# Kernel optimization log

Measured on AMD Instinct MI355X. Metric: run time of the kernel, lower is better.

Reference implementation:

```python
import jax, jax.numpy as jnp
import numpy as np

D_MODEL = 1024
NUM_HEADS = 16
D_K = D_MODEL // NUM_HEADS


def setup_inputs() -> dict:
    key = jax.random.key(0)
    k_x, k_q, k_k, k_v, k_o = jax.random.split(key, 5)
    s = 1.0 / np.sqrt(D_MODEL)
    return {
        "x": jax.random.normal(k_x, (2, 2048, D_MODEL), dtype=jnp.float32),
        "W_q": jax.random.normal(k_q, (D_MODEL, D_MODEL), dtype=jnp.float32) * s,
        "W_k": jax.random.normal(k_k, (D_MODEL, D_MODEL), dtype=jnp.float32) * s,
        "W_v": jax.random.normal(k_v, (D_MODEL, D_MODEL), dtype=jnp.float32) * s,
        "W_o": jax.random.normal(k_o, (D_MODEL, D_MODEL), dtype=jnp.float32) * s,
    }


def reference(x, W_q, W_k, W_v, W_o):
    B, S, D = x.shape
    H, dk = NUM_HEADS, D_K
    # nn.Linear(y) = y @ W.T ; weights stored as (out, in)
    def proj(W):
        return (x @ W.T).reshape(B, S, H, dk).transpose(0, 2, 1, 3)  # (B,H,S,dk)
    Q, K, V = proj(W_q), proj(W_k), proj(W_v)
    scores = jnp.einsum("bhqd,bhkd->bhqk", Q, K) / np.sqrt(dk)  # (B,H,S,S)
    attn = jax.nn.softmax(scores, axis=-1)
    out = jnp.einsum("bhqk,bhkd->bhqd", attn, V)  # (B,H,S,dk)
    out = out.transpose(0, 2, 1, 3).reshape(B, S, D)
    return out @ W_o.T
```

## Files before the change

kernel.cpp:

```cpp
#include <hip/hip_runtime.h>
#include <hip/hip_bf16.h>

#define SEQ 2048
#define DM  1024
#define NH  16
#define DK  64
#define MROWS 4096

typedef __attribute__((ext_vector_type(8))) short short8;
typedef __attribute__((ext_vector_type(4))) short short4v;
typedef __attribute__((ext_vector_type(4))) float float4v;

__device__ __forceinline__ short f2bf(float f) {
  union { float f; unsigned u; } v; v.f = f;
  unsigned r = v.u + 0x7fffu + ((v.u >> 16) & 1u);
  return (short)(r >> 16);
}
__device__ __forceinline__ short f2bfu(float f) {
  union { float f; unsigned u; } v; v.f = f;
  return (short)((v.u + 0x8000u) >> 16);
}

__global__ __launch_bounds__(256) void cvt_kernel(
    const float* __restrict__ in, short* __restrict__ out) {
  int i = blockIdx.x * 256 + threadIdx.x;
  float4v f = ((const float4v*)in)[i];
  short4v s;
#pragma unroll
  for (int j = 0; j < 4; ++j) s[j] = f2bf(f[j]);
  ((short4v*)out)[i] = s;
}

__global__ __launch_bounds__(256) void cvt4_kernel(
    const float* __restrict__ a, const float* __restrict__ b,
    const float* __restrict__ c, const float* __restrict__ d,
    short* __restrict__ out) {
  const float* srcs[4] = {a, b, c, d};
  const float* s = srcs[blockIdx.y];
  int i = blockIdx.x * 256 + threadIdx.x;
  float4v f = ((const float4v*)s)[i];
  short4v sv;
#pragma unroll
  for (int j = 0; j < 4; ++j) sv[j] = f2bf(f[j]);
  ((short4v*)(out + (size_t)blockIdx.y * DM * DM))[i] = sv;
}

template<typename TC>
__global__ __launch_bounds__(256) void gemm_bt_kernel(
    const short* __restrict__ A, const short* __restrict__ Bw0,
    TC* __restrict__ C0, int M, int N, int K, size_t strB, size_t strC,
    short* __restrict__ vtOut)
{
  __shared__ __align__(16) short Al[2][128 * 72];
  __shared__ __align__(16) short Bl[2][128 * 72];
  const short* Bw = Bw0 + (size_t)blockIdx.z * strB;
  TC* C = C0 + (size_t)blockIdx.z * strC;

  const int tid  = threadIdx.x;
  const int lane = tid & 63, wave = tid >> 6;
  const int l16  = lane & 15, quad = lane >> 4;
  const int wm   = (wave >> 1) * 64, wn = (wave & 1) * 64;
  const int cm   = blockIdx.y * 128, cn = blockIdx.x * 128;

  float4v acc[4][4];
#pragma unroll
  for (int i = 0; i < 4; ++i)
#pragma unroll
    for (int j = 0; j < 4; ++j)
#pragma unroll
      for (int r = 0; r < 4; ++r) acc[i][j][r] = 0.f;

  const short* ag = A  + (size_t)cm * K;
  const short* bg = Bw + (size_t)cn * K;
  int rw[4];
#pragma unroll
  for (int it = 0; it < 4; ++it) rw[it] = (it * 256 + tid) >> 3;
  const int cl = (tid & 7) * 8;

  short8 ra[4], rb[4];
  auto loadG = [&](int k0) {
#pragma unroll
    for (int it = 0; it < 4; ++it) {
      ra[it] = *(const short8*)(ag + (size_t)rw[it] * K + k0 + cl);
      rb[it] = *(const short8*)(bg + (size_t)rw[it] * K + k0 + cl);
    }
  };
  auto writeL = [&](int buf) {
#pragma unroll
    for (int it = 0; it < 4; ++it) {
      *(short8*)&Al[buf][rw[it] * 72 + cl] = ra[it];
      *(short8*)&Bl[buf][rw[it] * 72 + cl] = rb[it];
    }
  };
  auto compute = [&](int buf) {
#pragma unroll
    for (int ks = 0; ks < 2; ++ks) {
      short8 af[4], bfr[4];
#pragma unroll
      for (int mi = 0; mi < 4; ++mi)
        af[mi] = *(const short8*)&Al[buf][(wm + mi*16 + l16) * 72 + ks*32 + quad*8];
#pragma unroll
      for (int ni = 0; ni < 4; ++ni)
        bfr[ni] = *(const short8*)&Bl[buf][(wn + ni*16 + l16) * 72 + ks*32 + quad*8];
#pragma unroll
      for (int mi = 0; mi < 4; ++mi)
#pragma unroll
        for (int ni = 0; ni < 4; ++ni)
          acc[mi][ni] = __builtin_amdgcn_mfma_f32_16x16x32_bf16(
              af[mi], bfr[ni], acc[mi][ni], 0, 0, 0);
    }
  };

  loadG(0);
  writeL(0);
  __syncthreads();
  int cur = 0;
  for (int k0 = 0; k0 < K; k0 += 64) {
    bool nxt = (k0 + 64 < K);
    if (nxt) loadG(k0 + 64);
    compute(cur);
    if (nxt) writeL(cur ^ 1);
    __syncthreads();
    cur ^= 1;
  }

  if (vtOut != nullptr && blockIdx.z == 2) {
    short* T = &Al[0][0];
#pragma unroll
    for (int mi = 0; mi < 4; ++mi)
#pragma unroll
      for (int ni = 0; ni < 4; ++ni)
#pragma unroll
        for (int r = 0; r < 4; ++r)
          T[(wn + ni*16 + l16) * 136 + wm + mi*16 + quad*4 + r] =
              f2bf(acc[mi][ni][r]);
    __syncthreads();
    const int nrow = tid >> 1, mo = (tid & 1) * 64;
    const int b = cm >> 11;
    const int s0 = (cm & (SEQ - 1)) + mo;
    short* vt = vtOut + ((size_t)b * DM + cn + nrow) * SEQ + s0;
#pragma unroll
    for (int j = 0; j < 8; ++j)
      *(short8*)(vt + j * 8) = *(const short8*)&T[nrow * 136 + mo + j * 8];
  } else {
#pragma unroll
    for (int mi = 0; mi < 4; ++mi)
#pragma unroll
      for (int ni = 0; ni < 4; ++ni)
#pragma unroll
        for (int r = 0; r < 4; ++r) {
          int m = cm + wm + mi*16 + quad*4 + r;
          int n = cn + wn + ni*16 + l16;
          float v = acc[mi][ni][r];
          if constexpr (sizeof(TC) == 2) C[(size_t)m * N + n] = f2bf(v);
          else                           C[(size_t)m * N + n] = v;
        }
  }
}

__global__ __launch_bounds__(256) void flash_kernel(
    const short* __restrict__ Q, const short* __restrict__ Kg,
    const short* __restrict__ VTg, short* __restrict__ AO)
{
  __shared__ __align__(16) short Kl[2][64 * 72];
  __shared__ __align__(16) short Vt[2][64 * 72];
  __shared__ __align__(16) short Pl[4][32 * 72];
  __shared__ float lsumL[4][32];
  const int tid  = threadIdx.x;
  const int lane = tid & 63, wave = tid >> 6;
  const int l16  = lane & 15, quad = lane >> 4;
  const int q0   = blockIdx.x * 128;
  const int hc   = blockIdx.y * DK;
  const size_t base = (size_t)blockIdx.z * SEQ;

  short8 qfr[2][2];
#pragma unroll
  for (int qf = 0; qf < 2; ++qf)
#pragma unroll
    for (int ks = 0; ks < 2; ++ks)
      qfr[qf][ks] = *(const short8*)(Q + (base + q0 + wave*32 + qf*16 + l16) * DM
                                     + hc + ks*32 + quad*8);

  float4v O[2][4];
  float lsum[2] = {0.f, 0.f};
#pragma unroll
  for (int mt = 0; mt < 2; ++mt)
#pragma unroll
    for (int nt = 0; nt < 4; ++nt)
#pragma unroll
      for (int r = 0; r < 4; ++r) O[mt][nt][r] = 0.f;

  const float sc = 0.18033688011112042f;

  const int r0 = tid >> 3, r1 = (256 + tid) >> 3;
  const int c0 = (tid & 7) * 8;
  const short* vtb = VTg + ((size_t)blockIdx.z * DM + hc) * SEQ;

  short8 ka0, ka1, va0, va1;
  auto loadKV = [&](int kb) {
    ka0 = *(const short8*)(Kg + (base + kb*64 + r0) * DM + hc + c0);
    ka1 = *(const short8*)(Kg + (base + kb*64 + r1) * DM + hc + c0);
    va0 = *(const short8*)(vtb + (size_t)r0 * SEQ + kb*64 + c0);
    va1 = *(const short8*)(vtb + (size_t)r1 * SEQ + kb*64 + c0);
  };
  auto writeKV = [&](int buf) {
    *(short8*)&Kl[buf][r0 * 72 + c0] = ka0;
    *(short8*)&Kl[buf][r1 * 72 + c0] = ka1;
    *(short8*)&Vt[buf][r0 * 72 + c0] = va0;
    *(short8*)&Vt[buf][r1 * 72 + c0] = va1;
  };

  loadKV(0);
  writeKV(0);
  __syncthreads();

  int cur = 0;
  for (int kb = 0; kb < SEQ / 64; ++kb) {
    bool nxt = (kb + 1 < SEQ / 64);
    if (nxt) loadKV(kb + 1);

    float4v s[4][2];
#pragma unroll
    for (int kf = 0; kf < 4; ++kf)
#pragma unroll
      for (int qf = 0; qf < 2; ++qf)
#pragma unroll
        for (int r = 0; r < 4; ++r) s[kf][qf][r] = 0.f;
#pragma unroll
    for (int ks = 0; ks < 2; ++ks) {
#pragma unroll
      for (int kf = 0; kf < 4; ++kf) {
        short8 kfr = *(const short8*)&Kl[cur][(kf*16 + l16) * 72 + ks*32 + quad*8];
#pragma unroll
        for (int qf = 0; qf < 2; ++qf)
          s[kf][qf] = __builtin_amdgcn_mfma_f32_16x16x32_bf16(
              kfr, qfr[qf][ks], s[kf][qf], 0, 0, 0);
      }
    }
#pragma unroll
    for (int kf = 0; kf < 4; ++kf)
#pragma unroll
      for (int qf = 0; qf < 2; ++qf) {
        float p0 = exp2f(s[kf][qf][0] * sc), p1 = exp2f(s[kf][qf][1] * sc);
        float p2 = exp2f(s[kf][qf][2] * sc), p3 = exp2f(s[kf][qf][3] * sc);
        lsum[qf] += (p0 + p1) + (p2 + p3);
        short4v pk;
        pk[0] = f2bfu(p0); pk[1] = f2bfu(p1); pk[2] = f2bfu(p2); pk[3] = f2bfu(p3);
        *(short4v*)&Pl[wave][(qf*16 + l16) * 72 + kf*16 + quad*4] = pk;
      }
#pragma unroll
    for (int ks = 0; ks < 2; ++ks) {
      short8 pf[2];
#pragma unroll
      for (int mt = 0; mt < 2; ++mt)
        pf[mt] = *(const short8*)&Pl[wave][(mt*16 + l16) * 72 + ks*32 + quad*8];
#pragma unroll
      for (int nt = 0; nt < 4; ++nt) {
        short8 vf = *(const short8*)&Vt[cur][(nt*16 + l16) * 72 + ks*32 + quad*8];
#pragma unroll
        for (int mt = 0; mt < 2; ++mt)
          O[mt][nt] = __builtin_amdgcn_mfma_f32_16x16x32_bf16(
              pf[mt], vf, O[mt][nt], 0, 0, 0);
      }
    }
    if (nxt) writeKV(cur ^ 1);
    __syncthreads();
    cur ^= 1;
  }

#pragma unroll
  for (int qf = 0; qf < 2; ++qf) {
    float l = lsum[qf];
    l += __shfl_xor(l, 16, 64);
    l += __shfl_xor(l, 32, 64);
    lsumL[wave][qf*16 + l16] = l;
  }
#pragma unroll
  for (int mt = 0; mt < 2; ++mt) {
    float inv[4];
#pragma unroll
    for (int r = 0; r < 4; ++r)
      inv[r] = 1.f / lsumL[wave][mt*16 + quad*4 + r];
#pragma unroll
    for (int nt = 0; nt < 4; ++nt)
#pragma unroll
      for (int r = 0; r < 4; ++r) {
        int m = q0 + wave*32 + mt*16 + quad*4 + r;
        AO[(base + m) * DM + hc + nt*16 + l16] = f2bf(O[mt][nt][r] * inv[r]);
      }
  }
}

extern "C" void kernel_launch(void* const* d_in, const int* in_sizes, int n_in,
                              void* d_out, int out_size, void* d_ws, size_t ws_size,
                              hipStream_t stream) {
  (void)in_sizes; (void)n_in; (void)out_size; (void)ws_size;
  const float* x  = (const float*)d_in[0];
  const float* Wq = (const float*)d_in[1];
  const float* Wk = (const float*)d_in[2];
  const float* Wv = (const float*)d_in[3];
  const float* Wo = (const float*)d_in[4];
  float* out = (float*)d_out;

  const size_t NX = (size_t)MROWS * DM;
  const size_t NW = (size_t)DM * DM;
  short* xb  = (short*)d_ws;
  short* Wqb = xb  + NX;
  short* Qb  = Wqb + 4 * NW;
  short* Kb  = Qb  + NX;
  short* AO  = Kb  + NX;
  short* VTb = AO  + NX;

  cvt_kernel<<<dim3(NX / 4 / 256), 256, 0, stream>>>(x, xb);
  cvt4_kernel<<<dim3(NW / 4 / 256, 4), 256, 0, stream>>>(Wq, Wk, Wv, Wo, Wqb);

  gemm_bt_kernel<short><<<dim3(DM / 128, MROWS / 128, 3), 256, 0, stream>>>(
      xb, Wqb, Qb, MROWS, DM, DM, NW, NX, VTb);

  flash_kernel<<<dim3(SEQ / 128, NH, 2), 256, 0, stream>>>(Qb, Kb, VTb, AO);

  gemm_bt_kernel<float><<<dim3(DM / 128, MROWS / 128, 1), 256, 0, stream>>>(
      AO, Wqb + 3 * NW, out, MROWS, DM, DM, 0, 0, nullptr);
}
```

Measured before the change: 214.7 us.

## Templatize GEMM tiles, single-buffer LDS, fold softmax scale into Q projection

The GEMM becomes a template over the wave grid, drops the double-buffered LDS for a single buffer with an extra barrier, and sets launch bounds to allow 3 blocks per CU. The output projection switches to 64x128 tiles with 128 threads to launch more blocks. The softmax scale (log2e/sqrt(dk)) is folded into the Q projection epilogue, which removes a multiply per score in the flash kernel. The flash kernel also uses the hardware exp2 builtin and a perm-based bf16 pack, and seeds the QK MFMA chain from zero. Risks: bf16 rounding of the pre-scaled Q slightly changes numerics, and the single LDS buffer serializes global-to-LDS writes with compute.

```diff
diff --git a/kernel.cpp b/kernel.cpp
--- a/kernel.cpp
+++ b/kernel.cpp
@@ -10,15 +10,28 @@
 typedef __attribute__((ext_vector_type(8))) short short8;
 typedef __attribute__((ext_vector_type(4))) short short4v;
 typedef __attribute__((ext_vector_type(4))) float float4v;
+typedef __attribute__((ext_vector_type(2))) unsigned uint2v;
 
 __device__ __forceinline__ short f2bf(float f) {
   union { float f; unsigned u; } v; v.f = f;
   unsigned r = v.u + 0x7fffu + ((v.u >> 16) & 1u);
   return (short)(r >> 16);
 }
-__device__ __forceinline__ short f2bfu(float f) {
-  union { float f; unsigned u; } v; v.f = f;
-  return (short)((v.u + 0x8000u) >> 16);
+
+#if __has_builtin(__builtin_amdgcn_exp2f)
+#define EXP2(x) __builtin_amdgcn_exp2f(x)
+#else
+#define EXP2(x) exp2f(x)
+#endif
+
+__device__ __forceinline__ unsigned pack_bfu(float a, float b) {
+  unsigned ua = __float_as_uint(a) + 0x8000u;
+  unsigned ub = __float_as_uint(b) + 0x8000u;
+#if __has_builtin(__builtin_amdgcn_perm)
+  return __builtin_amdgcn_perm(ub, ua, 0x07060302u);
+#else
+  return (ua >> 16) | (ub & 0xffff0000u);
+#endif
 }
 
 __global__ __launch_bounds__(256) void cvt_kernel(
@@ -45,22 +58,28 @@
   ((short4v*)(out + (size_t)blockIdx.y * DM * DM))[i] = sv;
 }
 
-template<typename TC>
-__global__ __launch_bounds__(256) void gemm_bt_kernel(
+template<int WM, int WN, typename TC>
+__global__ __launch_bounds__(WM*WN*64, 3) void gemm_bt(
     const short* __restrict__ A, const short* __restrict__ Bw0,
     TC* __restrict__ C0, int M, int N, int K, size_t strB, size_t strC,
-    short* __restrict__ vtOut)
+    short* __restrict__ vtOut, float qs0)
 {
-  __shared__ __align__(16) short Al[2][128 * 72];
-  __shared__ __align__(16) short Bl[2][128 * 72];
+  constexpr int THREADS = WM * WN * 64;
+  constexpr int TM = WM * 64, TN = WN * 64;
+  constexpr int CA = TM * 64 / (8 * THREADS);
+  constexpr int CB = TN * 64 / (8 * THREADS);
+  __shared__ __align__(16) short SMEM[(TM + TN) * 72];
+  short* Al = SMEM;
+  short* Bl = SMEM + TM * 72;
+
   const short* Bw = Bw0 + (size_t)blockIdx.z * strB;
   TC* C = C0 + (size_t)blockIdx.z * strC;
 
   const int tid  = threadIdx.x;
   const int lane = tid & 63, wave = tid >> 6;
   const int l16  = lane & 15, quad = lane >> 4;
-  const int wm   = (wave >> 1) * 64, wn = (wave & 1) * 64;
-  const int cm   = blockIdx.y * 128, cn = blockIdx.x * 128;
+  const int wm   = (wave / WN) * 64, wn = (wave % WN) * 64;
+  const int cm   = blockIdx.y * TM, cn = blockIdx.x * TN;
 
   float4v acc[4][4];
 #pragma unroll
@@ -72,36 +91,38 @@
 
   const short* ag = A  + (size_t)cm * K;
   const short* bg = Bw + (size_t)cn * K;
-  int rw[4];
-#pragma unroll
-  for (int it = 0; it < 4; ++it) rw[it] = (it * 256 + tid) >> 3;
+  int rwa[CA], rwb[CB];
+#pragma unroll
+  for (int i = 0; i < CA; ++i) rwa[i] = (i * THREADS + tid) >> 3;
+#pragma unroll
+  for (int i = 0; i < CB; ++i) rwb[i] = (i * THREADS + tid) >> 3;
   const int cl = (tid & 7) * 8;
 
-  short8 ra[4], rb[4];
+  short8 ra[CA], rb[CB];
   auto loadG = [&](int k0) {
 #pragma unroll
-    for (int it = 0; it < 4; ++it) {
-      ra[it] = *(const short8*)(ag + (size_t)rw[it] * K + k0 + cl);
-      rb[it] = *(const short8*)(bg + (size_t)rw[it] * K + k0 + cl);
-    }
-  };
-  auto writeL = [&](int buf) {
-#pragma unroll
-    for (int it = 0; it < 4; ++it) {
-      *(short8*)&Al[buf][rw[it] * 72 + cl] = ra[it];
-      *(short8*)&Bl[buf][rw[it] * 72 + cl] = rb[it];
-    }
-  };
-  auto compute = [&](int buf) {
+    for (int i = 0; i < CA; ++i)
+      ra[i] = *(const short8*)(ag + (size_t)rwa[i] * K + k0 + cl);
+#pragma unroll
+    for (int i = 0; i < CB; ++i)
+      rb[i] = *(const short8*)(bg + (size_t)rwb[i] * K + k0 + cl);
+  };
+  auto writeL = [&]() {
+#pragma unroll
+    for (int i = 0; i < CA; ++i) *(short8*)&Al[rwa[i] * 72 + cl] = ra[i];
+#pragma unroll
+    for (int i = 0; i < CB; ++i) *(short8*)&Bl[rwb[i] * 72 + cl] = rb[i];
+  };
+  auto compute = [&]() {
 #pragma unroll
     for (int ks = 0; ks < 2; ++ks) {
       short8 af[4], bfr[4];
 #pragma unroll
       for (int mi = 0; mi < 4; ++mi)
-        af[mi] = *(const short8*)&Al[buf][(wm + mi*16 + l16) * 72 + ks*32 + quad*8];
+        af[mi] = *(const short8*)&Al[(wm + mi*16 + l16) * 72 + ks*32 + quad*8];
 #pragma unroll
       for (int ni = 0; ni < 4; ++ni)
-        bfr[ni] = *(const short8*)&Bl[buf][(wn + ni*16 + l16) * 72 + ks*32 + quad*8];
+        bfr[ni] = *(const short8*)&Bl[(wn + ni*16 + l16) * 72 + ks*32 + quad*8];
 #pragma unroll
       for (int mi = 0; mi < 4; ++mi)
 #pragma unroll
@@ -112,50 +133,52 @@
   };
 
   loadG(0);
-  writeL(0);
+  writeL();
   __syncthreads();
-  int cur = 0;
   for (int k0 = 0; k0 < K; k0 += 64) {
     bool nxt = (k0 + 64 < K);
     if (nxt) loadG(k0 + 64);
-    compute(cur);
-    if (nxt) writeL(cur ^ 1);
+    compute();
     __syncthreads();
-    cur ^= 1;
-  }
-
-  if (vtOut != nullptr && blockIdx.z == 2) {
-    short* T = &Al[0][0];
-#pragma unroll
-    for (int mi = 0; mi < 4; ++mi)
-#pragma unroll
-      for (int ni = 0; ni < 4; ++ni)
-#pragma unroll
-        for (int r = 0; r < 4; ++r)
-          T[(wn + ni*16 + l16) * 136 + wm + mi*16 + quad*4 + r] =
-              f2bf(acc[mi][ni][r]);
-    __syncthreads();
-    const int nrow = tid >> 1, mo = (tid & 1) * 64;
-    const int b = cm >> 11;
-    const int s0 = (cm & (SEQ - 1)) + mo;
-    short* vt = vtOut + ((size_t)b * DM + cn + nrow) * SEQ + s0;
-#pragma unroll
-    for (int j = 0; j < 8; ++j)
-      *(short8*)(vt + j * 8) = *(const short8*)&T[nrow * 136 + mo + j * 8];
-  } else {
-#pragma unroll
-    for (int mi = 0; mi < 4; ++mi)
-#pragma unroll
-      for (int ni = 0; ni < 4; ++ni)
-#pragma unroll
-        for (int r = 0; r < 4; ++r) {
-          int m = cm + wm + mi*16 + quad*4 + r;
-          int n = cn + wn + ni*16 + l16;
-          float v = acc[mi][ni][r];
-          if constexpr (sizeof(TC) == 2) C[(size_t)m * N + n] = f2bf(v);
-          else                           C[(size_t)m * N + n] = v;
-        }
-  }
+    if (nxt) { writeL(); __syncthreads(); }
+  }
+
+  const float scl = (blockIdx.z == 0) ? qs0 : 1.f;
+
+  if constexpr (WM == 2 && WN == 2) {
+    if (vtOut != nullptr && blockIdx.z == 2) {
+      short* T = SMEM;
+#pragma unroll
+      for (int mi = 0; mi < 4; ++mi)
+#pragma unroll
+        for (int ni = 0; ni < 4; ++ni)
+#pragma unroll
+          for (int r = 0; r < 4; ++r)
+            T[(wn + ni*16 + l16) * 136 + wm + mi*16 + quad*4 + r] =
+                f2bf(acc[mi][ni][r]);
+      __syncthreads();
+      const int nrow = tid >> 1, mo = (tid & 1) * 64;
+      const int b = cm >> 11;
+      const int s0 = (cm & (SEQ - 1)) + mo;
+      short* vt = vtOut + ((size_t)b * DM + cn + nrow) * SEQ + s0;
+#pragma unroll
+      for (int j = 0; j < 8; ++j)
+        *(short8*)(vt + j * 8) = *(const short8*)&T[nrow * 136 + mo + j * 8];
+      return;
+    }
+  }
+#pragma unroll
+  for (int mi = 0; mi < 4; ++mi)
+#pragma unroll
+    for (int ni = 0; ni < 4; ++ni)
+#pragma unroll
+      for (int r = 0; r < 4; ++r) {
+        int m = cm + wm + mi*16 + quad*4 + r;
+        int n = cn + wn + ni*16 + l16;
+        float v = acc[mi][ni][r] * scl;
+        if constexpr (sizeof(TC) == 2) C[(size_t)m * N + n] = f2bf(v);
+        else                           C[(size_t)m * N + n] = v;
+      }
 }
 
 __global__ __launch_bounds__(256) void flash_kernel(
@@ -190,7 +213,7 @@
 #pragma unroll
       for (int r = 0; r < 4; ++r) O[mt][nt][r] = 0.f;
 
-  const float sc = 0.18033688011112042f;
+  const float4v z4 = {0.f, 0.f, 0.f, 0.f};
 
   const int r0 = tid >> 3, r1 = (256 + tid) >> 3;
   const int c0 = (tid & 7) * 8;
@@ -221,32 +244,26 @@
 
     float4v s[4][2];
 #pragma unroll
+    for (int kf = 0; kf < 4; ++kf) {
+      short8 k0 = *(const short8*)&Kl[cur][(kf*16 + l16) * 72 + quad*8];
+      short8 k1 = *(const short8*)&Kl[cur][(kf*16 + l16) * 72 + 32 + quad*8];
+#pragma unroll
+      for (int qf = 0; qf < 2; ++qf) {
+        float4v t = __builtin_amdgcn_mfma_f32_16x16x32_bf16(k0, qfr[qf][0], z4, 0, 0, 0);
+        s[kf][qf]  = __builtin_amdgcn_mfma_f32_16x16x32_bf16(k1, qfr[qf][1], t, 0, 0, 0);
+      }
+    }
+#pragma unroll
     for (int kf = 0; kf < 4; ++kf)
 #pragma unroll
-      for (int qf = 0; qf < 2; ++qf)
-#pragma unroll
-        for (int r = 0; r < 4; ++r) s[kf][qf][r] = 0.f;
-#pragma unroll
-    for (int ks = 0; ks < 2; ++ks) {
-#pragma unroll
-      for (int kf = 0; kf < 4; ++kf) {
-        short8 kfr = *(const short8*)&Kl[cur][(kf*16 + l16) * 72 + ks*32 + quad*8];
-#pragma unroll
-        for (int qf = 0; qf < 2; ++qf)
-          s[kf][qf] = __builtin_amdgcn_mfma_f32_16x16x32_bf16(
-              kfr, qfr[qf][ks], s[kf][qf], 0, 0, 0);
-      }
-    }
-#pragma unroll
-    for (int kf = 0; kf < 4; ++kf)
-#pragma unroll
       for (int qf = 0; qf < 2; ++qf) {
-        float p0 = exp2f(s[kf][qf][0] * sc), p1 = exp2f(s[kf][qf][1] * sc);
-        float p2 = exp2f(s[kf][qf][2] * sc), p3 = exp2f(s[kf][qf][3] * sc);
+        float p0 = EXP2(s[kf][qf][0]), p1 = EXP2(s[kf][qf][1]);
+        float p2 = EXP2(s[kf][qf][2]), p3 = EXP2(s[kf][qf][3]);
         lsum[qf] += (p0 + p1) + (p2 + p3);
-        short4v pk;
-        pk[0] = f2bfu(p0); pk[1] = f2bfu(p1); pk[2] = f2bfu(p2); pk[3] = f2bfu(p3);
-        *(short4v*)&Pl[wave][(qf*16 + l16) * 72 + kf*16 + quad*4] = pk;
+        uint2v pk;
+        pk[0] = pack_bfu(p0, p1);
+        pk[1] = pack_bfu(p2, p3);
+        *(uint2v*)&Pl[wave][(qf*16 + l16) * 72 + kf*16 + quad*4] = pk;
       }
 #pragma unroll
     for (int ks = 0; ks < 2; ++ks) {
@@ -314,11 +331,13 @@
   cvt_kernel<<<dim3(NX / 4 / 256), 256, 0, stream>>>(x, xb);
   cvt4_kernel<<<dim3(NW / 4 / 256, 4), 256, 0, stream>>>(Wq, Wk, Wv, Wo, Wqb);
 
-  gemm_bt_kernel<short><<<dim3(DM / 128, MROWS / 128, 3), 256, 0, stream>>>(
-      xb, Wqb, Qb, MROWS, DM, DM, NW, NX, VTb);
+  const float qs = 0.18033688011112042f;
+
+  gemm_bt<2, 2, short><<<dim3(DM / 128, MROWS / 128, 3), 256, 0, stream>>>(
+      xb, Wqb, Qb, MROWS, DM, DM, NW, NX, VTb, qs);
 
   flash_kernel<<<dim3(SEQ / 128, NH, 2), 256, 0, stream>>>(Qb, Kb, VTb, AO);
 
-  gemm_bt_kernel<float><<<dim3(DM / 128, MROWS / 128, 1), 256, 0, stream>>>(
-      AO, Wqb + 3 * NW, out, MROWS, DM, DM, 0, 0, nullptr);
-}
+  gemm_bt<1, 2, float><<<dim3(DM / 128, MROWS / 64, 1), 128, 0, stream>>>(
+      AO, Wqb + 3 * NW, out, MROWS, DM, DM, 0, 0, nullptr, 1.f);
+}
```

Result: faster. 203.4 us (-5.3%).
